# Performance work log

Hardware: AMD Instinct MI355X
Metric: run time of the kernel (lower is better)

Reference implementation:

```python
import jax, jax.numpy as jnp
import numpy as np

STRIDE, PAD, DIL = 1, 1, 1


def setup_inputs() -> dict:
    key = jax.random.key(0)
    k1, k2, k3, k4, k5 = jax.random.split(key, 5)
    B, C, W = 16, 256, 4096
    OC, K = 256, 3
    x = jax.random.normal(k1, (B, C, W), jnp.float32)
    weight = jax.random.normal(k2, (OC, C, K), jnp.float32) * 0.05
    offset = jax.random.normal(k3, (B, K, W), jnp.float32)  # offset_groups = 1
    mask = jax.random.uniform(k4, (B, K, W), jnp.float32)   # modulation in [0,1)
    bias = jax.random.normal(k5, (OC,), jnp.float32) * 0.05
    return {"x": x, "weight": weight, "offset": offset, "mask": mask, "bias": bias}


def _deform_conv1d(x, weight, offset, mask, bias):
    B, C, Win = x.shape
    OC, Cg, K = weight.shape
    Wout = offset.shape[-1]
    G = offset.shape[1] // K       # offset groups
    NG = C // Cg                   # weight groups
    Cpg = C // G                   # channels per offset group

    # sampling positions: p[b,g,k,w] = w*stride - pad + k*dil + offset
    base = jnp.arange(Wout, dtype=x.dtype) * STRIDE - PAD      # [Wout]
    kpos = jnp.arange(K, dtype=x.dtype) * DIL                  # [K]
    p = base[None, None, None, :] + kpos[None, None, :, None] \
        + offset.reshape(B, G, K, Wout)                        # [B,G,K,Wout]

    p0f = jnp.floor(p)
    w1 = p - p0f
    w0 = 1.0 - w1
    i0 = p0f.astype(jnp.int32)
    i1 = i0 + 1

    xg = x.reshape(B, G, Cpg, 1, Win)  # broadcastable over kernel axis

    def gather(idx):
        valid = (idx >= 0) & (idx < Win)                        # [B,G,K,Wout]
        idxc = jnp.clip(idx, 0, Win - 1)[:, :, None, :, :]      # [B,G,1,K,Wout]
        v = jnp.take_along_axis(xg, idxc, axis=-1)              # [B,G,Cpg,K,Wout]
        return jnp.where(valid[:, :, None], v, 0.0)

    sampled = gather(i0) * w0[:, :, None] + gather(i1) * w1[:, :, None]
    sampled = sampled * mask.reshape(B, G, 1, K, Wout)          # modulated (v2)

    # grouped contraction
    s = sampled.reshape(B, NG, Cg, K, Wout)                     # [B,NG,Cg,K,Wout]
    wg = weight.reshape(NG, OC // NG, Cg, K)                    # [NG,OCg,Cg,K]
    out = jnp.einsum('bgckw,gock->bgow', s, wg).reshape(B, OC, Wout)
    return out + bias[None, :, None]


def reference(x, weight, offset, mask, bias):
    return _deform_conv1d(x, weight, offset, mask, bias)
```

## Files before the change

### kernel.cpp

```cpp
#include <hip/hip_runtime.h>

#define BATCH 16
#define CCH   256
#define WLEN  4096
#define OCH   256
#define KW    3
#define CK    768
#define WIN   96
#define CHUNK 32
#define NCHUNK 8
#define SLD   104

typedef short bf16x8 __attribute__((ext_vector_type(8)));
typedef short bf16x4 __attribute__((ext_vector_type(4)));
typedef float f32x4  __attribute__((ext_vector_type(4)));

__device__ inline short f2bf(float f) {
    union { float f; unsigned u; } v; v.f = f;
    unsigned r = v.u + 0x7FFFu + ((v.u >> 16) & 1u);
    return (short)(r >> 16);
}

__device__ inline void gl_lds16(const void* g, void* l) {
    __builtin_amdgcn_global_load_lds(
        (const __attribute__((address_space(1))) unsigned int*)g,
        (__attribute__((address_space(3))) unsigned int*)l, 16, 0, 0);
}

__global__ void wconv_kernel(const float* __restrict__ w, short* __restrict__ wb) {
    int i = blockIdx.x * 256 + threadIdx.x;
    wb[i] = f2bf(w[i]);
}

__global__ __launch_bounds__(512, 4)
void deform_fused_kernel(const float* __restrict__ x,
                         const short* __restrict__ wb,
                         const float* __restrict__ off,
                         const float* __restrict__ msk,
                         const float* __restrict__ bias,
                         float* __restrict__ out) {
    __shared__ float WinS[2][CHUNK * WIN];
    __shared__ short SlS[2][64 * SLD];

    const int t      = threadIdx.x;
    const int b      = blockIdx.x >> 6;
    const int wt     = blockIdx.x & 63;
    const int lane   = t & 63;
    const int wv     = t >> 6;
    const int lr     = lane & 15;
    const int lq     = lane >> 4;
    const int wstart = wt * 64 - 16;
    const int wg     = wt * 64 + lane;

    int   li[3];
    float rw0[3], rw1[3];
#pragma unroll
    for (int k = 0; k < 3; ++k) {
        float o  = off[b * (KW * WLEN) + k * WLEN + wg];
        float m  = msk[b * (KW * WLEN) + k * WLEN + wg];
        float p  = (float)(wg - 1 + k) + o;
        float pf = floorf(p);
        float w1 = p - pf;
        int i0 = (int)pf;
        int i1 = i0 + 1;
        bool v0 = (i0 >= 0) & (i0 < WLEN);
        bool v1 = (i1 >= 0) & (i1 < WLEN);
        li[k]  = min(max(i0 - wstart, 0), WIN - 2);
        rw0[k] = v0 ? m * (1.0f - w1) : 0.0f;
        rw1[k] = v1 ? m * w1 : 0.0f;
    }

    const float* xb = x + (size_t)b * CCH * WLEN;

    const int sA = t;
    const int chA = sA / 24, oA = sA - chA * 24;
    const int jA  = min(max(wstart + oA * 4, 0), WLEN - 4);
    const int offA = chA * WLEN + jA;
    const int sB = 512 + t;
    const int chB = sB / 24, oB = sB - chB * 24;
    const int jB  = min(max(wstart + oB * 4, 0), WLEN - 4);
    const int offB = chB * WLEN + jB;

    f32x4 acc[2][4];
#pragma unroll
    for (int i = 0; i < 2; ++i)
#pragma unroll
        for (int j = 0; j < 4; ++j)
            acc[i][j] = (f32x4){0.f, 0.f, 0.f, 0.f};

    auto stage = [&](int c, int bufsel) {
        const float* src = xb + (size_t)c * CHUNK * WLEN;
        gl_lds16(src + offA, &WinS[bufsel][wv * 256]);
        if (wv < 4) gl_lds16(src + offB, &WinS[bufsel][2048 + wv * 256]);
    };

    auto gather = [&](int bufsel) {
        short obuf[12];
#pragma unroll
        for (int dc = 0; dc < 4; ++dc) {
            const float* row = &WinS[bufsel][(wv * 4 + dc) * WIN];
#pragma unroll
            for (int k = 0; k < 3; ++k) {
                float v0 = row[li[k]];
                float v1 = row[li[k] + 1];
                obuf[dc * 3 + k] = f2bf(rw0[k] * v0 + rw1[k] * v1);
            }
        }
        short* sp = &SlS[bufsel][lane * SLD + wv * 12];
#pragma unroll
        for (int j = 0; j < 3; ++j)
            *reinterpret_cast<bf16x4*>(sp + j * 4) =
                *reinterpret_cast<const bf16x4*>(&obuf[j * 4]);
    };

    auto mfma_chunk = [&](int c, int bufsel) {
#pragma unroll
        for (int ks = 0; ks < 3; ++ks) {
            bf16x8 af[2], bfv[4];
#pragma unroll
            for (int mt = 0; mt < 2; ++mt)
                af[mt] = *reinterpret_cast<const bf16x8*>(
                    wb + (size_t)(wv * 32 + mt * 16 + lr) * CK + c * 96 + ks * 32 + lq * 8);
#pragma unroll
            for (int nt = 0; nt < 4; ++nt)
                bfv[nt] = *reinterpret_cast<const bf16x8*>(
                    &SlS[bufsel][(nt * 16 + lr) * SLD + ks * 32 + lq * 8]);
#pragma unroll
            for (int mt = 0; mt < 2; ++mt)
#pragma unroll
                for (int nt = 0; nt < 4; ++nt)
                    acc[mt][nt] = __builtin_amdgcn_mfma_f32_16x16x32_bf16(
                        af[mt], bfv[nt], acc[mt][nt], 0, 0, 0);
        }
    };

    stage(0, 0);
    __syncthreads();
    stage(1, 1);
    gather(0);
    __syncthreads();

#pragma unroll 2
    for (int c = 0; c < NCHUNK; ++c) {
        if (c < NCHUNK - 2) stage(c + 2, c & 1);
        if (c < NCHUNK - 1) gather((c + 1) & 1);
        mfma_chunk(c, c & 1);
        if (c < NCHUNK - 1) __syncthreads();
    }

    float* ob = out + ((size_t)b * OCH) * WLEN + wt * 64;
#pragma unroll
    for (int mt = 0; mt < 2; ++mt) {
#pragma unroll
        for (int r = 0; r < 4; ++r) {
            int row = wv * 32 + mt * 16 + lq * 4 + r;
            float bv = bias[row];
            float* orow = ob + (size_t)row * WLEN + lr;
#pragma unroll
            for (int nt = 0; nt < 4; ++nt)
                orow[nt * 16] = acc[mt][nt][r] + bv;
        }
    }
}

extern "C" void kernel_launch(void* const* d_in, const int* in_sizes, int n_in,
                              void* d_out, int out_size, void* d_ws, size_t ws_size,
                              hipStream_t stream) {
    const float* x    = (const float*)d_in[0];
    const float* w    = (const float*)d_in[1];
    const float* off  = (const float*)d_in[2];
    const float* msk  = (const float*)d_in[3];
    const float* bias = (const float*)d_in[4];
    float* out = (float*)d_out;
    short* wb  = (short*)d_ws;

    wconv_kernel<<<768, 256, 0, stream>>>(w, wb);
    deform_fused_kernel<<<BATCH * 64, 512, 0, stream>>>(x, wb, off, msk, bias, out);
}
```

Before: 163.9 us.

## Triple-buffer input staging with explicit vmcnt waits and MFMA priority

Moves the x-window staging from double to triple buffering so loads run three chunks ahead. The loop is fully unrolled and uses manual s_waitcnt vmcnt/lgkmcnt waits plus raw s_barrier instead of __syncthreads, so a barrier waits only for the oldest outstanding load. It also raises wave priority around the MFMA bursts. This adds LDS use, which may lower occupancy, and the hand-counted vmcnt values are fragile if the compiler reorders or adds memory ops.

```diff
diff --git a/kernel.cpp b/kernel.cpp
--- a/kernel.cpp
+++ b/kernel.cpp
@@ -27,6 +27,14 @@
         (__attribute__((address_space(3))) unsigned int*)l, 16, 0, 0);
 }
 
+template<int N> __device__ inline void vmwait() {
+    if constexpr (N == 0)      asm volatile("s_waitcnt vmcnt(0)" ::: "memory");
+    else if constexpr (N == 1) asm volatile("s_waitcnt vmcnt(1)" ::: "memory");
+    else if constexpr (N == 2) asm volatile("s_waitcnt vmcnt(2)" ::: "memory");
+    else if constexpr (N == 4) asm volatile("s_waitcnt vmcnt(4)" ::: "memory");
+}
+__device__ inline void lgkm0() { asm volatile("s_waitcnt lgkmcnt(0)" ::: "memory"); }
+
 __global__ void wconv_kernel(const float* __restrict__ w, short* __restrict__ wb) {
     int i = blockIdx.x * 256 + threadIdx.x;
     wb[i] = f2bf(w[i]);
@@ -39,7 +47,7 @@
                          const float* __restrict__ msk,
                          const float* __restrict__ bias,
                          float* __restrict__ out) {
-    __shared__ float WinS[2][CHUNK * WIN];
+    __shared__ float WinS[3][CHUNK * WIN];
     __shared__ short SlS[2][64 * SLD];
 
     const int t      = threadIdx.x;
@@ -94,11 +102,11 @@
         if (wv < 4) gl_lds16(src + offB, &WinS[bufsel][2048 + wv * 256]);
     };
 
-    auto gather = [&](int bufsel) {
+    auto gather = [&](int wbuf, int sbuf) {
         short obuf[12];
 #pragma unroll
         for (int dc = 0; dc < 4; ++dc) {
-            const float* row = &WinS[bufsel][(wv * 4 + dc) * WIN];
+            const float* row = &WinS[wbuf][(wv * 4 + dc) * WIN];
 #pragma unroll
             for (int k = 0; k < 3; ++k) {
                 float v0 = row[li[k]];
@@ -106,14 +114,14 @@
                 obuf[dc * 3 + k] = f2bf(rw0[k] * v0 + rw1[k] * v1);
             }
         }
-        short* sp = &SlS[bufsel][lane * SLD + wv * 12];
+        short* sp = &SlS[sbuf][lane * SLD + wv * 12];
 #pragma unroll
         for (int j = 0; j < 3; ++j)
             *reinterpret_cast<bf16x4*>(sp + j * 4) =
                 *reinterpret_cast<const bf16x4*>(&obuf[j * 4]);
     };
 
-    auto mfma_chunk = [&](int c, int bufsel) {
+    auto mfma_chunk = [&](int c, int sbuf) {
 #pragma unroll
         for (int ks = 0; ks < 3; ++ks) {
             bf16x8 af[2], bfv[4];
@@ -124,29 +132,55 @@
 #pragma unroll
             for (int nt = 0; nt < 4; ++nt)
                 bfv[nt] = *reinterpret_cast<const bf16x8*>(
-                    &SlS[bufsel][(nt * 16 + lr) * SLD + ks * 32 + lq * 8]);
+                    &SlS[sbuf][(nt * 16 + lr) * SLD + ks * 32 + lq * 8]);
+            __builtin_amdgcn_s_setprio(1);
 #pragma unroll
             for (int mt = 0; mt < 2; ++mt)
 #pragma unroll
                 for (int nt = 0; nt < 4; ++nt)
                     acc[mt][nt] = __builtin_amdgcn_mfma_f32_16x16x32_bf16(
                         af[mt], bfv[nt], acc[mt][nt], 0, 0, 0);
+            __builtin_amdgcn_s_setprio(0);
         }
     };
 
     stage(0, 0);
-    __syncthreads();
     stage(1, 1);
-    gather(0);
-    __syncthreads();
-
-#pragma unroll 2
-    for (int c = 0; c < NCHUNK; ++c) {
-        if (c < NCHUNK - 2) stage(c + 2, c & 1);
-        if (c < NCHUNK - 1) gather((c + 1) & 1);
-        mfma_chunk(c, c & 1);
-        if (c < NCHUNK - 1) __syncthreads();
-    }
+    stage(2, 2);
+    if (wv < 4) vmwait<4>(); else vmwait<2>();
+    __builtin_amdgcn_s_barrier();
+    gather(0, 0);
+
+#define ITER_FULL(c)                                                  \
+    if (wv < 4) vmwait<2>(); else vmwait<1>();     \
+    lgkm0();                                                          \
+    __builtin_amdgcn_s_barrier();                                     \
+    stage((c) + 3, (c) % 3);                                          \
+    gather(((c) + 1) % 3, ((c) + 1) & 1);                             \
+    mfma_chunk((c), (c) & 1);
+
+    ITER_FULL(0)
+    ITER_FULL(1)
+    ITER_FULL(2)
+    ITER_FULL(3)
+    ITER_FULL(4)
+#undef ITER_FULL
+
+    if (wv < 4) vmwait<2>(); else vmwait<1>();
+    lgkm0();
+    __builtin_amdgcn_s_barrier();
+    gather(0, 0);
+    mfma_chunk(5, 1);
+
+    vmwait<0>();
+    lgkm0();
+    __builtin_amdgcn_s_barrier();
+    gather(1, 1);
+    mfma_chunk(6, 0);
+
+    lgkm0();
+    __builtin_amdgcn_s_barrier();
+    mfma_chunk(7, 1);
 
     float* ob = out + ((size_t)b * OCH) * WLEN + wt * 64;
 #pragma unroll
```

Result: no change. 162.2 us (-1.0%).

## Gather deformable samples directly from global memory instead of LDS-staged windows

Applied to the files above, without the earlier changes.

Removes the global_load_lds staging of a 96-wide x window per channel chunk and has each lane load its two interpolation taps straight from global memory (relying on cache), cutting the LDS footprint. With less LDS, launch bounds are raised to target six blocks per CU, the chunk loop is fully unrolled, and MFMA sections are wrapped in s_setprio to favor the matrix issue. The cost is scattered per-lane global loads with higher latency and no explicit double-buffered prefetch, plus a barrier every iteration.

```diff
diff --git a/kernel.cpp b/kernel.cpp
--- a/kernel.cpp
+++ b/kernel.cpp
@@ -6,7 +6,6 @@
 #define OCH   256
 #define KW    3
 #define CK    768
-#define WIN   96
 #define CHUNK 32
 #define NCHUNK 8
 #define SLD   104
@@ -21,25 +20,18 @@
     return (short)(r >> 16);
 }
 
-__device__ inline void gl_lds16(const void* g, void* l) {
-    __builtin_amdgcn_global_load_lds(
-        (const __attribute__((address_space(1))) unsigned int*)g,
-        (__attribute__((address_space(3))) unsigned int*)l, 16, 0, 0);
-}
-
 __global__ void wconv_kernel(const float* __restrict__ w, short* __restrict__ wb) {
     int i = blockIdx.x * 256 + threadIdx.x;
     wb[i] = f2bf(w[i]);
 }
 
-__global__ __launch_bounds__(512, 4)
+__global__ __launch_bounds__(512, 6)
 void deform_fused_kernel(const float* __restrict__ x,
                          const short* __restrict__ wb,
                          const float* __restrict__ off,
                          const float* __restrict__ msk,
                          const float* __restrict__ bias,
                          float* __restrict__ out) {
-    __shared__ float WinS[2][CHUNK * WIN];
     __shared__ short SlS[2][64 * SLD];
 
     const int t      = threadIdx.x;
@@ -49,10 +41,9 @@
     const int wv     = t >> 6;
     const int lr     = lane & 15;
     const int lq     = lane >> 4;
-    const int wstart = wt * 64 - 16;
     const int wg     = wt * 64 + lane;
 
-    int   li[3];
+    int   gb0[3], gb1[3];
     float rw0[3], rw1[3];
 #pragma unroll
     for (int k = 0; k < 3; ++k) {
@@ -65,21 +56,13 @@
         int i1 = i0 + 1;
         bool v0 = (i0 >= 0) & (i0 < WLEN);
         bool v1 = (i1 >= 0) & (i1 < WLEN);
-        li[k]  = min(max(i0 - wstart, 0), WIN - 2);
+        gb0[k] = min(max(i0, 0), WLEN - 1) * 4;
+        gb1[k] = min(max(i1, 0), WLEN - 1) * 4;
         rw0[k] = v0 ? m * (1.0f - w1) : 0.0f;
         rw1[k] = v1 ? m * w1 : 0.0f;
     }
 
     const float* xb = x + (size_t)b * CCH * WLEN;
-
-    const int sA = t;
-    const int chA = sA / 24, oA = sA - chA * 24;
-    const int jA  = min(max(wstart + oA * 4, 0), WLEN - 4);
-    const int offA = chA * WLEN + jA;
-    const int sB = 512 + t;
-    const int chB = sB / 24, oB = sB - chB * 24;
-    const int jB  = min(max(wstart + oB * 4, 0), WLEN - 4);
-    const int offB = chB * WLEN + jB;
 
     f32x4 acc[2][4];
 #pragma unroll
@@ -88,32 +71,26 @@
         for (int j = 0; j < 4; ++j)
             acc[i][j] = (f32x4){0.f, 0.f, 0.f, 0.f};
 
-    auto stage = [&](int c, int bufsel) {
-        const float* src = xb + (size_t)c * CHUNK * WLEN;
-        gl_lds16(src + offA, &WinS[bufsel][wv * 256]);
-        if (wv < 4) gl_lds16(src + offB, &WinS[bufsel][2048 + wv * 256]);
-    };
-
-    auto gather = [&](int bufsel) {
+    auto gather = [&](int c, int sbuf) {
         short obuf[12];
 #pragma unroll
         for (int dc = 0; dc < 4; ++dc) {
-            const float* row = &WinS[bufsel][(wv * 4 + dc) * WIN];
+            const char* xrow = (const char*)(xb + (size_t)(c * CHUNK + wv * 4 + dc) * WLEN);
 #pragma unroll
             for (int k = 0; k < 3; ++k) {
-                float v0 = row[li[k]];
-                float v1 = row[li[k] + 1];
+                float v0 = *(const float*)(xrow + gb0[k]);
+                float v1 = *(const float*)(xrow + gb1[k]);
                 obuf[dc * 3 + k] = f2bf(rw0[k] * v0 + rw1[k] * v1);
             }
         }
-        short* sp = &SlS[bufsel][lane * SLD + wv * 12];
+        short* sp = &SlS[sbuf][lane * SLD + wv * 12];
 #pragma unroll
         for (int j = 0; j < 3; ++j)
             *reinterpret_cast<bf16x4*>(sp + j * 4) =
                 *reinterpret_cast<const bf16x4*>(&obuf[j * 4]);
     };
 
-    auto mfma_chunk = [&](int c, int bufsel) {
+    auto mfma_chunk = [&](int c, int sbuf) {
 #pragma unroll
         for (int ks = 0; ks < 3; ++ks) {
             bf16x8 af[2], bfv[4];
@@ -124,28 +101,25 @@
 #pragma unroll
             for (int nt = 0; nt < 4; ++nt)
                 bfv[nt] = *reinterpret_cast<const bf16x8*>(
-                    &SlS[bufsel][(nt * 16 + lr) * SLD + ks * 32 + lq * 8]);
+                    &SlS[sbuf][(nt * 16 + lr) * SLD + ks * 32 + lq * 8]);
+            __builtin_amdgcn_s_setprio(1);
 #pragma unroll
             for (int mt = 0; mt < 2; ++mt)
 #pragma unroll
                 for (int nt = 0; nt < 4; ++nt)
                     acc[mt][nt] = __builtin_amdgcn_mfma_f32_16x16x32_bf16(
                         af[mt], bfv[nt], acc[mt][nt], 0, 0, 0);
+            __builtin_amdgcn_s_setprio(0);
         }
     };
 
-    stage(0, 0);
+    gather(0, 0);
     __syncthreads();
-    stage(1, 1);
-    gather(0);
-    __syncthreads();
-
-#pragma unroll 2
+#pragma unroll
     for (int c = 0; c < NCHUNK; ++c) {
-        if (c < NCHUNK - 2) stage(c + 2, c & 1);
-        if (c < NCHUNK - 1) gather((c + 1) & 1);
+        if (c < NCHUNK - 1) gather(c + 1, (c + 1) & 1);
         mfma_chunk(c, c & 1);
-        if (c < NCHUNK - 1) __syncthreads();
+        __syncthreads();
     }
 
     float* ob = out + ((size_t)b * OCH) * WLEN + wt * 64;
```

Result: slower. 317.1 us (+93.5%).
